# Performance work log

Hardware: AMD Instinct MI355X
Metric: run time of the kernel (lower is better)

The kernel has to match this reference:

```python
import jax, jax.numpy as jnp
import numpy as np

N = 50000      # nodes
E = 800000     # edges in normalized A (incl. self loops)
DIN = 128      # input_dim
DOUT = 64      # output_dim
BN_EPS = 1e-5
SLOPE = 0.01   # LeakyReLU default negative slope


def setup_inputs() -> dict:
    key = jax.random.key(0)
    ks = jax.random.split(key, 10)
    H = jax.random.normal(ks[0], (N, DIN), dtype=jnp.float32)
    rows = jax.random.randint(ks[1], (E,), 0, N, dtype=jnp.int32)
    cols = jax.random.randint(ks[2], (E,), 0, N, dtype=jnp.int32)
    # values of the symmetrically normalized adjacency (precomputed in __init__)
    vals = jax.random.uniform(ks[3], (E,), dtype=jnp.float32)
    # BatchNorm1d params/buffers (eval mode: use running stats)
    gamma = 1.0 + 0.1 * jax.random.normal(ks[4], (DIN,), dtype=jnp.float32)
    beta = 0.1 * jax.random.normal(ks[5], (DIN,), dtype=jnp.float32)
    run_mean = 0.1 * jax.random.normal(ks[6], (DIN,), dtype=jnp.float32)
    run_var = 0.5 + jax.random.uniform(ks[7], (DIN,), dtype=jnp.float32)
    # Linear(input_dim, output_dim)
    W = jax.random.normal(ks[8], (DIN, DOUT), dtype=jnp.float32) / np.sqrt(DIN)
    b = 0.01 * jax.random.normal(ks[9], (DOUT,), dtype=jnp.float32)
    return dict(H=H, rows=rows, cols=cols, vals=vals, gamma=gamma, beta=beta,
                run_mean=run_mean, run_var=run_var, W=W, b=b)


def reference(H, rows, cols, vals, gamma, beta, run_mean, run_var, W, b):
    # F.normalize: L2 row normalization with eps=1e-12
    norm = jnp.maximum(jnp.linalg.norm(H, axis=1, keepdims=True), 1e-12)
    Hn = H / norm
    # BatchNorm1d (eval: running stats); dropout is identity in eval
    scale = gamma * jax.lax.rsqrt(run_var + BN_EPS)
    Hb = (Hn - run_mean) * scale + beta
    # Linear projection [N, DIN] @ [DIN, DOUT]
    X = Hb @ W + b
    # SpMM: out[r] = sum_{e: rows[e]==r} vals[e] * X[cols[e]]
    msgs = vals[:, None] * X[cols]            # [E, DOUT] gather + scale
    out = jax.ops.segment_sum(msgs, rows, num_segments=N)
    # LeakyReLU
    return jnp.where(out >= 0, out, SLOPE * out)
```

## Files before the change

### kernel.cpp

```cpp
#include <hip/hip_runtime.h>
#include <hip/hip_fp16.h>

#define N_NODES 50000
#define E_EDGES 800000
#define DIN 128
#define DOUT 64
#define NBUK 196
#define BUKCAP 4608
#define CHUNK 2048
#define NBLKA 391
#define ASTRIDE 136

typedef short short8 __attribute__((ext_vector_type(8)));
typedef float f32x4 __attribute__((ext_vector_type(4)));

static __device__ __forceinline__ short f2bf(float f)
{
    union { float f; unsigned u; } x{f};
    const unsigned r = x.u + 0x7FFFu + ((x.u >> 16) & 1u);
    return (short)(r >> 16);
}

__global__ __launch_bounds__(256) void k_x(
    const float* __restrict__ H, const float* __restrict__ gamma,
    const float* __restrict__ beta, const float* __restrict__ mean,
    const float* __restrict__ var, const float* __restrict__ W,
    const float* __restrict__ bias, unsigned short* __restrict__ X16,
    int* __restrict__ gcursor)
{
    __shared__ short A_s[64][ASTRIDE];
    __shared__ short B_s[64][ASTRIDE];
    const int t = threadIdx.x;
    const int l = t & 63, wv = t >> 6;
    const int R0 = blockIdx.x * 64;

    if (blockIdx.x == 0 && t < NBUK) gcursor[t] = 0;

    {
        const int n = t >> 2, koff = (t & 3) * 32;
#pragma unroll
        for (int i = 0; i < 16; ++i) {
            const int k = koff + i * 2;
            const unsigned lo = (unsigned short)f2bf(W[k * DOUT + n]);
            const unsigned hi = (unsigned short)f2bf(W[(k + 1) * DOUT + n]);
            *(unsigned*)&B_s[n][k] = lo | (hi << 16);
        }
    }
    {
        const int rloc = t >> 2, sub = t & 3;
        const int r = R0 + rloc;
        float4 h[8];
        if (r < N_NODES) {
            const float4* hp = (const float4*)(H + (size_t)r * DIN + sub * 32);
#pragma unroll
            for (int i = 0; i < 8; ++i) h[i] = hp[i];
        } else {
#pragma unroll
            for (int i = 0; i < 8; ++i) h[i] = make_float4(0.f, 0.f, 0.f, 0.f);
        }
        float ss = 0.f;
#pragma unroll
        for (int i = 0; i < 8; ++i)
            ss += h[i].x * h[i].x + h[i].y * h[i].y + h[i].z * h[i].z + h[i].w * h[i].w;
        ss += __shfl_xor(ss, 1, 64);
        ss += __shfl_xor(ss, 2, 64);
        const float inv = 1.0f / fmaxf(sqrtf(ss), 1e-12f);

        const float4* gp = (const float4*)(gamma + sub * 32);
        const float4* bp = (const float4*)(beta  + sub * 32);
        const float4* mp = (const float4*)(mean  + sub * 32);
        const float4* vp = (const float4*)(var   + sub * 32);
#pragma unroll
        for (int i = 0; i < 8; ++i) {
            const float4 g4 = gp[i], b4 = bp[i], m4 = mp[i], v4 = vp[i];
            const float s0 = g4.x * rsqrtf(v4.x + 1e-5f);
            const float s1 = g4.y * rsqrtf(v4.y + 1e-5f);
            const float s2 = g4.z * rsqrtf(v4.z + 1e-5f);
            const float s3 = g4.w * rsqrtf(v4.w + 1e-5f);
            const float e0 = h[i].x * inv * s0 + (b4.x - m4.x * s0);
            const float e1 = h[i].y * inv * s1 + (b4.y - m4.y * s1);
            const float e2 = h[i].z * inv * s2 + (b4.z - m4.z * s2);
            const float e3 = h[i].w * inv * s3 + (b4.w - m4.w * s3);
            const unsigned u0 = (unsigned short)f2bf(e0) | ((unsigned)(unsigned short)f2bf(e1) << 16);
            const unsigned u1 = (unsigned short)f2bf(e2) | ((unsigned)(unsigned short)f2bf(e3) << 16);
            *(uint2*)&A_s[rloc][sub * 32 + i * 4] = make_uint2(u0, u1);
        }
    }

    const int ml = l & 15, q = l >> 4;
    f32x4 c0, c1, c2, c3;
    {
        const float b0 = bias[ml],      b1 = bias[16 + ml];
        const float b2 = bias[32 + ml], b3 = bias[48 + ml];
        c0 = f32x4{b0, b0, b0, b0};
        c1 = f32x4{b1, b1, b1, b1};
        c2 = f32x4{b2, b2, b2, b2};
        c3 = f32x4{b3, b3, b3, b3};
    }
    __syncthreads();

#pragma unroll
    for (int k0 = 0; k0 < 4; ++k0) {
        const short8 a  = *(const short8*)&A_s[wv * 16 + ml][k0 * 32 + q * 8];
        const short8 b0 = *(const short8*)&B_s[ml][k0 * 32 + q * 8];
        const short8 b1 = *(const short8*)&B_s[16 + ml][k0 * 32 + q * 8];
        const short8 b2 = *(const short8*)&B_s[32 + ml][k0 * 32 + q * 8];
        const short8 b3 = *(const short8*)&B_s[48 + ml][k0 * 32 + q * 8];
        c0 = __builtin_amdgcn_mfma_f32_16x16x32_bf16(a, b0, c0, 0, 0, 0);
        c1 = __builtin_amdgcn_mfma_f32_16x16x32_bf16(a, b1, c1, 0, 0, 0);
        c2 = __builtin_amdgcn_mfma_f32_16x16x32_bf16(a, b2, c2, 0, 0, 0);
        c3 = __builtin_amdgcn_mfma_f32_16x16x32_bf16(a, b3, c3, 0, 0, 0);
    }

    __syncthreads();
    unsigned short* otile = (unsigned short*)&A_s[0][0];
#pragma unroll
    for (int i = 0; i < 4; ++i) {
        const int r = wv * 16 + q * 4 + i;
        otile[r * 64 + ml]      = __half_as_ushort(__float2half(c0[i]));
        otile[r * 64 + 16 + ml] = __half_as_ushort(__float2half(c1[i]));
        otile[r * 64 + 32 + ml] = __half_as_ushort(__float2half(c2[i]));
        otile[r * 64 + 48 + ml] = __half_as_ushort(__float2half(c3[i]));
    }
    __syncthreads();
#pragma unroll
    for (int rep = 0; rep < 2; ++rep) {
        const int id = rep * 256 + t;
        const int row = id >> 3;
        const int off = (id & 7) * 8;
        if (R0 + row < N_NODES)
            *(uint4*)(X16 + (size_t)(R0 + row) * DOUT + off) =
                *(const uint4*)&otile[row * 64 + off];
    }
}

__global__ __launch_bounds__(512) void k_passA(
    const int* __restrict__ rows, const int* __restrict__ cols,
    const float* __restrict__ vals, int* __restrict__ gcursor,
    unsigned* __restrict__ midVC, unsigned char* __restrict__ midR)
{
    __shared__ int lhist[NBUK], lstart[NBUK], lcur[NBUK], gbase[NBUK];
    __shared__ int scn[256];
    __shared__ unsigned lbinVC[CHUNK];
    __shared__ unsigned short lbinBR[CHUNK];
    const int t = threadIdx.x;
    const int e0 = blockIdx.x * CHUNK;
    const int nC = min(CHUNK, E_EDGES - e0);

    if (t < NBUK) lhist[t] = 0;
    __syncthreads();

    unsigned prVC[4];
    unsigned short prBR[4];
#pragma unroll
    for (int k = 0; k < 4; ++k) {
        const int e = e0 + k * 512 + t;
        if (e < E_EDGES) {
            const int r = rows[e];
            const unsigned hv = __half_as_ushort(__float2half(vals[e]));
            prVC[k] = (hv << 16) | (unsigned)cols[e];
            prBR[k] = (unsigned short)r;
            atomicAdd(&lhist[r >> 8], 1);
        } else {
            prBR[k] = 0xFFFFu;
        }
    }
    __syncthreads();

    const int v = (t < NBUK) ? lhist[t] : 0;
    if (t < 256) scn[t] = v;
    __syncthreads();
    for (int o = 1; o < 256; o <<= 1) {
        int u = 0;
        if (t < 256 && t >= o) u = scn[t - o];
        __syncthreads();
        if (t < 256) scn[t] += u;
        __syncthreads();
    }
    if (t < NBUK) {
        const int ex = scn[t] - v;
        lstart[t] = ex;
        lcur[t] = ex;
        gbase[t] = t * BUKCAP + (v ? atomicAdd(&gcursor[t], v) : 0);
    }
    __syncthreads();

#pragma unroll
    for (int k = 0; k < 4; ++k) {
        if (prBR[k] != 0xFFFFu) {
            const int bk = prBR[k] >> 8;
            const int pos = atomicAdd(&lcur[bk], 1);
            lbinVC[pos] = prVC[k];
            lbinBR[pos] = prBR[k];
        }
    }
    __syncthreads();

    for (int i = t; i < nC; i += 512) {
        const unsigned short br = lbinBR[i];
        const int bk = br >> 8;
        const int g = gbase[bk] + (i - lstart[bk]);
        if (g < (bk + 1) * BUKCAP) {
            midVC[g] = lbinVC[i];
            midR[g] = (unsigned char)(br & 255);
        }
    }
}

__global__ __launch_bounds__(512) void k_passB(
    const int* __restrict__ gcursor, const unsigned* __restrict__ midVC,
    const unsigned char* __restrict__ midR, unsigned* __restrict__ ev,
    int* __restrict__ rowS, int* __restrict__ rowE)
{
    __shared__ int lhist[256], scn[256], lcur[256];
    const int t = threadIdx.x;
    const int b = blockIdx.x;
    const int base = b * BUKCAP;
    const int total = min(gcursor[b], BUKCAP);

    if (t < 256) lhist[t] = 0;
    __syncthreads();
    for (int i = t; i < total; i += 512)
        atomicAdd(&lhist[midR[base + i]], 1);
    __syncthreads();

    const int v = (t < 256) ? lhist[t] : 0;
    if (t < 256) scn[t] = v;
    __syncthreads();
    for (int o = 1; o < 256; o <<= 1) {
        int u = 0;
        if (t < 256 && t >= o) u = scn[t - o];
        __syncthreads();
        if (t < 256) scn[t] += u;
        __syncthreads();
    }
    if (t < 256) {
        const int ex = scn[t] - v;
        lcur[t] = ex;
        const int gr = (b << 8) | t;
        if (gr < N_NODES) { rowS[gr] = base + ex; rowE[gr] = base + ex + v; }
    }
    __syncthreads();

    for (int i = t; i < total; i += 512) {
        const int lr = midR[base + i];
        const int pos = atomicAdd(&lcur[lr], 1);
        ev[base + pos] = midVC[base + i];
    }
}

__global__ __launch_bounds__(256) void k_spmm(
    const int* __restrict__ rowS, const int* __restrict__ rowE,
    const unsigned* __restrict__ ev, const unsigned short* __restrict__ X16,
    float* __restrict__ out)
{
    const int lane = threadIdx.x & 63;
    const int hl   = lane & 31;
    const int h    = lane >> 5;
    const int row  = blockIdx.x * 4 + (threadIdx.x >> 6);
    const int s  = rowS[row];
    const int e2 = rowE[row];
    float ax = 0.f, ay = 0.f;
    for (int c = s; c < e2; c += 64) {
        const int idx = c + lane;
        unsigned p = 0;
        if (idx < e2) p = ev[idx];
        const int cnt  = min(e2 - c, 64);
        const int jmax = (cnt + 1) >> 1;
        int j = 0;
        for (; j + 1 < jmax; j += 2) {
            const unsigned u0 = (unsigned)__shfl((int)p, 2 * j + h,     64);
            const unsigned u1 = (unsigned)__shfl((int)p, 2 * j + 2 + h, 64);
            const unsigned x0 = *(const unsigned*)(X16 + (u0 & 0xFFFFu) * DOUT + 2 * hl);
            const unsigned x1 = *(const unsigned*)(X16 + (u1 & 0xFFFFu) * DOUT + 2 * hl);
            const float v0 = __half2float(__ushort_as_half((unsigned short)(u0 >> 16)));
            const float v1 = __half2float(__ushort_as_half((unsigned short)(u1 >> 16)));
            const float2 f0 = __half22float2(*(const __half2*)&x0);
            const float2 f1 = __half22float2(*(const __half2*)&x1);
            ax = fmaf(v0, f0.x, ax); ay = fmaf(v0, f0.y, ay);
            ax = fmaf(v1, f1.x, ax); ay = fmaf(v1, f1.y, ay);
        }
        for (; j < jmax; ++j) {
            const unsigned u = (unsigned)__shfl((int)p, 2 * j + h, 64);
            const unsigned x = *(const unsigned*)(X16 + (u & 0xFFFFu) * DOUT + 2 * hl);
            const float v = __half2float(__ushort_as_half((unsigned short)(u >> 16)));
            const float2 f = __half22float2(*(const __half2*)&x);
            ax = fmaf(v, f.x, ax); ay = fmaf(v, f.y, ay);
        }
    }
    ax += __shfl_xor(ax, 32, 64);
    ay += __shfl_xor(ay, 32, 64);
    if (h == 0) {
        float2 r;
        r.x = (ax >= 0.f) ? ax : 0.01f * ax;
        r.y = (ay >= 0.f) ? ay : 0.01f * ay;
        *(float2*)(out + (size_t)row * DOUT + 2 * hl) = r;
    }
}

extern "C" void kernel_launch(void* const* d_in, const int* in_sizes, int n_in,
                              void* d_out, int out_size, void* d_ws, size_t ws_size,
                              hipStream_t stream)
{
    const float* H     = (const float*)d_in[0];
    const int*   rows  = (const int*)  d_in[1];
    const int*   cols  = (const int*)  d_in[2];
    const float* vals  = (const float*)d_in[3];
    const float* gamma = (const float*)d_in[4];
    const float* beta  = (const float*)d_in[5];
    const float* mean  = (const float*)d_in[6];
    const float* var   = (const float*)d_in[7];
    const float* W     = (const float*)d_in[8];
    const float* bias  = (const float*)d_in[9];
    float* out = (float*)d_out;

    char* ws = (char*)d_ws;
    unsigned short* X16     = (unsigned short*)(ws);
    int*            gcursor = (int*)          (ws +  6400000);
    unsigned*       midVC   = (unsigned*)     (ws +  6400800);
    unsigned char*  midR    = (unsigned char*)(ws + 10013472);
    unsigned*       ev      = (unsigned*)     (ws + 10916640);
    int*            rowS    = (int*)          (ws + 14529312);
    int*            rowE    = (int*)          (ws + 14730016);

    k_x<<<(N_NODES + 63) / 64, 256, 0, stream>>>(H, gamma, beta, mean, var, W,
                                                 bias, X16, gcursor);
    k_passA<<<NBLKA, 512, 0, stream>>>(rows, cols, vals, gcursor, midVC, midR);
    k_passB<<<NBUK, 512, 0, stream>>>(gcursor, midVC, midR, ev, rowS, rowE);
    k_spmm<<<N_NODES / 4, 256, 0, stream>>>(rowS, rowE, ev, X16, out);
}
```

Measured before the change: 158.1 us.

## Merge projection and edge bucketing into one launch; widen SpMM gathers

Fuses the dense projection kernel and the edge-bucketing pass into a single launch. The first block range does bucketing with 256 threads and eight edges per thread, the rest compute X, and a union of shared-memory layouts serves both. The bucket cursor reset moves to a memset, and the two independent stages can now overlap on the GPU, saving one launch. The SpMM kernel now has each lane gather four fp16 features (8 bytes), so four edges are processed per step instead of two, at the cost of an extra shuffle-reduction round.

```diff
diff --git a/kernel.cpp b/kernel.cpp
--- a/kernel.cpp
+++ b/kernel.cpp
@@ -9,6 +9,7 @@
 #define BUKCAP 4608
 #define CHUNK 2048
 #define NBLKA 391
+#define KXBLK 782
 #define ASTRIDE 136
 
 typedef short short8 __attribute__((ext_vector_type(8)));
@@ -21,20 +22,95 @@
     return (short)(r >> 16);
 }
 
-__global__ __launch_bounds__(256) void k_x(
+union SMemFront {
+    struct { short A[64][ASTRIDE]; short B[64][ASTRIDE]; } x;
+    struct {
+        int lhist[NBUK]; int lstart[NBUK]; int lcur[NBUK]; int gbase[NBUK];
+        int scn[256];
+        unsigned lbinVC[CHUNK];
+        unsigned short lbinBR[CHUNK];
+    } a;
+};
+
+__global__ __launch_bounds__(256) void k_front(
     const float* __restrict__ H, const float* __restrict__ gamma,
     const float* __restrict__ beta, const float* __restrict__ mean,
     const float* __restrict__ var, const float* __restrict__ W,
     const float* __restrict__ bias, unsigned short* __restrict__ X16,
-    int* __restrict__ gcursor)
-{
-    __shared__ short A_s[64][ASTRIDE];
-    __shared__ short B_s[64][ASTRIDE];
+    const int* __restrict__ rows, const int* __restrict__ cols,
+    const float* __restrict__ vals, int* __restrict__ gcursor,
+    unsigned* __restrict__ midVC, unsigned char* __restrict__ midR)
+{
+    __shared__ SMemFront sm;
     const int t = threadIdx.x;
+
+    if (blockIdx.x < NBLKA) {
+        const int e0 = blockIdx.x * CHUNK;
+        const int nC = min(CHUNK, E_EDGES - e0);
+
+        if (t < NBUK) sm.a.lhist[t] = 0;
+        __syncthreads();
+
+        unsigned prVC[8];
+        unsigned short prBR[8];
+#pragma unroll
+        for (int k = 0; k < 8; ++k) {
+            const int e = e0 + k * 256 + t;
+            if (e < E_EDGES) {
+                const int r = rows[e];
+                const unsigned hv = __half_as_ushort(__float2half(vals[e]));
+                prVC[k] = (hv << 16) | (unsigned)cols[e];
+                prBR[k] = (unsigned short)r;
+                atomicAdd(&sm.a.lhist[r >> 8], 1);
+            } else {
+                prBR[k] = 0xFFFFu;
+            }
+        }
+        __syncthreads();
+
+        const int v = (t < NBUK) ? sm.a.lhist[t] : 0;
+        sm.a.scn[t] = v;
+        __syncthreads();
+        for (int o = 1; o < 256; o <<= 1) {
+            int u = 0;
+            if (t >= o) u = sm.a.scn[t - o];
+            __syncthreads();
+            sm.a.scn[t] += u;
+            __syncthreads();
+        }
+        if (t < NBUK) {
+            const int ex = sm.a.scn[t] - v;
+            sm.a.lstart[t] = ex;
+            sm.a.lcur[t] = ex;
+            sm.a.gbase[t] = t * BUKCAP + (v ? atomicAdd(&gcursor[t], v) : 0);
+        }
+        __syncthreads();
+
+#pragma unroll
+        for (int k = 0; k < 8; ++k) {
+            if (prBR[k] != 0xFFFFu) {
+                const int bk = prBR[k] >> 8;
+                const int pos = atomicAdd(&sm.a.lcur[bk], 1);
+                sm.a.lbinVC[pos] = prVC[k];
+                sm.a.lbinBR[pos] = prBR[k];
+            }
+        }
+        __syncthreads();
+
+        for (int i = t; i < nC; i += 256) {
+            const unsigned short br = sm.a.lbinBR[i];
+            const int bk = br >> 8;
+            const int g = sm.a.gbase[bk] + (i - sm.a.lstart[bk]);
+            if (g < (bk + 1) * BUKCAP) {
+                midVC[g] = sm.a.lbinVC[i];
+                midR[g] = (unsigned char)(br & 255);
+            }
+        }
+        return;
+    }
+
     const int l = t & 63, wv = t >> 6;
-    const int R0 = blockIdx.x * 64;
-
-    if (blockIdx.x == 0 && t < NBUK) gcursor[t] = 0;
+    const int R0 = (blockIdx.x - NBLKA) * 64;
 
     {
         const int n = t >> 2, koff = (t & 3) * 32;
@@ -43,7 +119,7 @@
             const int k = koff + i * 2;
             const unsigned lo = (unsigned short)f2bf(W[k * DOUT + n]);
             const unsigned hi = (unsigned short)f2bf(W[(k + 1) * DOUT + n]);
-            *(unsigned*)&B_s[n][k] = lo | (hi << 16);
+            *(unsigned*)&sm.x.B[n][k] = lo | (hi << 16);
         }
     }
     {
@@ -83,7 +159,7 @@
             const float e3 = h[i].w * inv * s3 + (b4.w - m4.w * s3);
             const unsigned u0 = (unsigned short)f2bf(e0) | ((unsigned)(unsigned short)f2bf(e1) << 16);
             const unsigned u1 = (unsigned short)f2bf(e2) | ((unsigned)(unsigned short)f2bf(e3) << 16);
-            *(uint2*)&A_s[rloc][sub * 32 + i * 4] = make_uint2(u0, u1);
+            *(uint2*)&sm.x.A[rloc][sub * 32 + i * 4] = make_uint2(u0, u1);
         }
     }
 
@@ -101,11 +177,11 @@
 
 #pragma unroll
     for (int k0 = 0; k0 < 4; ++k0) {
-        const short8 a  = *(const short8*)&A_s[wv * 16 + ml][k0 * 32 + q * 8];
-        const short8 b0 = *(const short8*)&B_s[ml][k0 * 32 + q * 8];
-        const short8 b1 = *(const short8*)&B_s[16 + ml][k0 * 32 + q * 8];
-        const short8 b2 = *(const short8*)&B_s[32 + ml][k0 * 32 + q * 8];
-        const short8 b3 = *(const short8*)&B_s[48 + ml][k0 * 32 + q * 8];
+        const short8 a  = *(const short8*)&sm.x.A[wv * 16 + ml][k0 * 32 + q * 8];
+        const short8 b0 = *(const short8*)&sm.x.B[ml][k0 * 32 + q * 8];
+        const short8 b1 = *(const short8*)&sm.x.B[16 + ml][k0 * 32 + q * 8];
+        const short8 b2 = *(const short8*)&sm.x.B[32 + ml][k0 * 32 + q * 8];
+        const short8 b3 = *(const short8*)&sm.x.B[48 + ml][k0 * 32 + q * 8];
         c0 = __builtin_amdgcn_mfma_f32_16x16x32_bf16(a, b0, c0, 0, 0, 0);
         c1 = __builtin_amdgcn_mfma_f32_16x16x32_bf16(a, b1, c1, 0, 0, 0);
         c2 = __builtin_amdgcn_mfma_f32_16x16x32_bf16(a, b2, c2, 0, 0, 0);
@@ -113,7 +189,7 @@
     }
 
     __syncthreads();
-    unsigned short* otile = (unsigned short*)&A_s[0][0];
+    unsigned short* otile = (unsigned short*)&sm.x.A[0][0];
 #pragma unroll
     for (int i = 0; i < 4; ++i) {
         const int r = wv * 16 + q * 4 + i;
@@ -134,79 +210,6 @@
     }
 }
 
-__global__ __launch_bounds__(512) void k_passA(
-    const int* __restrict__ rows, const int* __restrict__ cols,
-    const float* __restrict__ vals, int* __restrict__ gcursor,
-    unsigned* __restrict__ midVC, unsigned char* __restrict__ midR)
-{
-    __shared__ int lhist[NBUK], lstart[NBUK], lcur[NBUK], gbase[NBUK];
-    __shared__ int scn[256];
-    __shared__ unsigned lbinVC[CHUNK];
-    __shared__ unsigned short lbinBR[CHUNK];
-    const int t = threadIdx.x;
-    const int e0 = blockIdx.x * CHUNK;
-    const int nC = min(CHUNK, E_EDGES - e0);
-
-    if (t < NBUK) lhist[t] = 0;
-    __syncthreads();
-
-    unsigned prVC[4];
-    unsigned short prBR[4];
-#pragma unroll
-    for (int k = 0; k < 4; ++k) {
-        const int e = e0 + k * 512 + t;
-        if (e < E_EDGES) {
-            const int r = rows[e];
-            const unsigned hv = __half_as_ushort(__float2half(vals[e]));
-            prVC[k] = (hv << 16) | (unsigned)cols[e];
-            prBR[k] = (unsigned short)r;
-            atomicAdd(&lhist[r >> 8], 1);
-        } else {
-            prBR[k] = 0xFFFFu;
-        }
-    }
-    __syncthreads();
-
-    const int v = (t < NBUK) ? lhist[t] : 0;
-    if (t < 256) scn[t] = v;
-    __syncthreads();
-    for (int o = 1; o < 256; o <<= 1) {
-        int u = 0;
-        if (t < 256 && t >= o) u = scn[t - o];
-        __syncthreads();
-        if (t < 256) scn[t] += u;
-        __syncthreads();
-    }
-    if (t < NBUK) {
-        const int ex = scn[t] - v;
-        lstart[t] = ex;
-        lcur[t] = ex;
-        gbase[t] = t * BUKCAP + (v ? atomicAdd(&gcursor[t], v) : 0);
-    }
-    __syncthreads();
-
-#pragma unroll
-    for (int k = 0; k < 4; ++k) {
-        if (prBR[k] != 0xFFFFu) {
-            const int bk = prBR[k] >> 8;
-            const int pos = atomicAdd(&lcur[bk], 1);
-            lbinVC[pos] = prVC[k];
-            lbinBR[pos] = prBR[k];
-        }
-    }
-    __syncthreads();
-
-    for (int i = t; i < nC; i += 512) {
-        const unsigned short br = lbinBR[i];
-        const int bk = br >> 8;
-        const int g = gbase[bk] + (i - lstart[bk]);
-        if (g < (bk + 1) * BUKCAP) {
-            midVC[g] = lbinVC[i];
-            midR[g] = (unsigned char)(br & 255);
-        }
-    }
-}
-
 __global__ __launch_bounds__(512) void k_passB(
     const int* __restrict__ gcursor, const unsigned* __restrict__ midVC,
     const unsigned char* __restrict__ midR, unsigned* __restrict__ ev,
@@ -255,46 +258,56 @@
     float* __restrict__ out)
 {
     const int lane = threadIdx.x & 63;
-    const int hl   = lane & 31;
-    const int h    = lane >> 5;
+    const int sub  = lane & 15;
+    const int g4   = lane >> 4;
     const int row  = blockIdx.x * 4 + (threadIdx.x >> 6);
     const int s  = rowS[row];
     const int e2 = rowE[row];
-    float ax = 0.f, ay = 0.f;
+    float a0 = 0.f, a1 = 0.f, a2 = 0.f, a3 = 0.f;
     for (int c = s; c < e2; c += 64) {
         const int idx = c + lane;
         unsigned p = 0;
         if (idx < e2) p = ev[idx];
         const int cnt  = min(e2 - c, 64);
-        const int jmax = (cnt + 1) >> 1;
+        const int jmax = (cnt + 3) >> 2;
         int j = 0;
         for (; j + 1 < jmax; j += 2) {
-            const unsigned u0 = (unsigned)__shfl((int)p, 2 * j + h,     64);
-            const unsigned u1 = (unsigned)__shfl((int)p, 2 * j + 2 + h, 64);
-            const unsigned x0 = *(const unsigned*)(X16 + (u0 & 0xFFFFu) * DOUT + 2 * hl);
-            const unsigned x1 = *(const unsigned*)(X16 + (u1 & 0xFFFFu) * DOUT + 2 * hl);
+            const unsigned u0 = (unsigned)__shfl((int)p, j * 4 + g4,     64);
+            const unsigned u1 = (unsigned)__shfl((int)p, j * 4 + 4 + g4, 64);
+            const uint2 x0 = *(const uint2*)(X16 + (u0 & 0xFFFFu) * DOUT + sub * 4);
+            const uint2 x1 = *(const uint2*)(X16 + (u1 & 0xFFFFu) * DOUT + sub * 4);
             const float v0 = __half2float(__ushort_as_half((unsigned short)(u0 >> 16)));
             const float v1 = __half2float(__ushort_as_half((unsigned short)(u1 >> 16)));
-            const float2 f0 = __half22float2(*(const __half2*)&x0);
-            const float2 f1 = __half22float2(*(const __half2*)&x1);
-            ax = fmaf(v0, f0.x, ax); ay = fmaf(v0, f0.y, ay);
-            ax = fmaf(v1, f1.x, ax); ay = fmaf(v1, f1.y, ay);
+            const float2 f00 = __half22float2(*(const __half2*)&x0.x);
+            const float2 f01 = __half22float2(*(const __half2*)&x0.y);
+            const float2 f10 = __half22float2(*(const __half2*)&x1.x);
+            const float2 f11 = __half22float2(*(const __half2*)&x1.y);
+            a0 = fmaf(v0, f00.x, a0); a1 = fmaf(v0, f00.y, a1);
+            a2 = fmaf(v0, f01.x, a2); a3 = fmaf(v0, f01.y, a3);
+            a0 = fmaf(v1, f10.x, a0); a1 = fmaf(v1, f10.y, a1);
+            a2 = fmaf(v1, f11.x, a2); a3 = fmaf(v1, f11.y, a3);
         }
         for (; j < jmax; ++j) {
-            const unsigned u = (unsigned)__shfl((int)p, 2 * j + h, 64);
-            const unsigned x = *(const unsigned*)(X16 + (u & 0xFFFFu) * DOUT + 2 * hl);
+            const unsigned u = (unsigned)__shfl((int)p, j * 4 + g4, 64);
+            const uint2 x = *(const uint2*)(X16 + (u & 0xFFFFu) * DOUT + sub * 4);
             const float v = __half2float(__ushort_as_half((unsigned short)(u >> 16)));
-            const float2 f = __half22float2(*(const __half2*)&x);
-            ax = fmaf(v, f.x, ax); ay = fmaf(v, f.y, ay);
-        }
-    }
-    ax += __shfl_xor(ax, 32, 64);
-    ay += __shfl_xor(ay, 32, 64);
-    if (h == 0) {
-        float2 r;
-        r.x = (ax >= 0.f) ? ax : 0.01f * ax;
-        r.y = (ay >= 0.f) ? ay : 0.01f * ay;
-        *(float2*)(out + (size_t)row * DOUT + 2 * hl) = r;
+            const float2 f0 = __half22float2(*(const __half2*)&x.x);
+            const float2 f1 = __half22float2(*(const __half2*)&x.y);
+            a0 = fmaf(v, f0.x, a0); a1 = fmaf(v, f0.y, a1);
+            a2 = fmaf(v, f1.x, a2); a3 = fmaf(v, f1.y, a3);
+        }
+    }
+    a0 += __shfl_xor(a0, 16, 64); a1 += __shfl_xor(a1, 16, 64);
+    a2 += __shfl_xor(a2, 16, 64); a3 += __shfl_xor(a3, 16, 64);
+    a0 += __shfl_xor(a0, 32, 64); a1 += __shfl_xor(a1, 32, 64);
+    a2 += __shfl_xor(a2, 32, 64); a3 += __shfl_xor(a3, 32, 64);
+    if (g4 == 0) {
+        float4 r;
+        r.x = (a0 >= 0.f) ? a0 : 0.01f * a0;
+        r.y = (a1 >= 0.f) ? a1 : 0.01f * a1;
+        r.z = (a2 >= 0.f) ? a2 : 0.01f * a2;
+        r.w = (a3 >= 0.f) ? a3 : 0.01f * a3;
+        *(float4*)(out + (size_t)row * DOUT + sub * 4) = r;
     }
 }
 
@@ -323,9 +336,11 @@
     int*            rowS    = (int*)          (ws + 14529312);
     int*            rowE    = (int*)          (ws + 14730016);
 
-    k_x<<<(N_NODES + 63) / 64, 256, 0, stream>>>(H, gamma, beta, mean, var, W,
-                                                 bias, X16, gcursor);
-    k_passA<<<NBLKA, 512, 0, stream>>>(rows, cols, vals, gcursor, midVC, midR);
+    hipMemsetAsync(gcursor, 0, NBUK * sizeof(int), stream);
+
+    k_front<<<NBLKA + KXBLK, 256, 0, stream>>>(H, gamma, beta, mean, var, W,
+                                               bias, X16, rows, cols, vals,
+                                               gcursor, midVC, midR);
     k_passB<<<NBUK, 512, 0, stream>>>(gcursor, midVC, midR, ev, rowS, rowE);
     k_spmm<<<N_NODES / 4, 256, 0, stream>>>(rowS, rowE, ev, X16, out);
 }
```

Result: faster. 148.5 us (-6.1%).
